# Optimization experiments

Measured on AMD Instinct MI355X. Metric: run time of the kernel, lower is better.

## Reference

```python
import jax, jax.numpy as jnp
import numpy as np

B, N, D, H, S = 4, 32768, 256, 8, 64
DH = D // H  # 32


def setup_inputs() -> dict:
    key = jax.random.key(0)
    ks = jax.random.split(key, 8)
    s = 0.02
    return {
        "x": jax.random.normal(ks[0], (B, N, D), jnp.float32),
        "W_fx": jax.random.normal(ks[1], (D, D), jnp.float32) * s,
        "b_fx": jnp.zeros((D,), jnp.float32),
        "W_x": jax.random.normal(ks[2], (D, D), jnp.float32) * s,
        "b_x": jnp.zeros((D,), jnp.float32),
        "W_slice": jax.random.normal(ks[3], (DH, S), jnp.float32) * s,
        "b_slice": jnp.zeros((S,), jnp.float32),
        "temperature": jnp.full((1, H, 1, 1), 0.5, jnp.float32),
        "W_qkv": jax.random.normal(ks[4], (DH, 3 * DH), jnp.float32) * s,  # qkv_bias=False
        "W_out": jax.random.normal(ks[5], (D, D), jnp.float32) * s,
        "b_out": jnp.zeros((D,), jnp.float32),
    }


def reference(x, W_fx, b_fx, W_x, b_x, W_slice, b_slice, temperature, W_qkv, W_out, b_out):
    b, n, d = x.shape
    h, dh = H, d // H
    scale = dh ** -0.5
    # per-head projections: [b, h, n, dh]
    fx_mid = (x @ W_fx + b_fx).reshape(b, n, h, dh).transpose(0, 2, 1, 3)
    x_mid = (x @ W_x + b_x).reshape(b, n, h, dh).transpose(0, 2, 1, 3)
    # soft slice assignment: softmax over slices [b, h, n, s]
    logits = (x_mid @ W_slice + b_slice) / temperature
    slice_weights = jax.nn.softmax(logits, axis=-1)
    slice_norm = slice_weights.sum(axis=2)  # [b, h, s]
    # weighted pooling of points into slice tokens [b, h, s, dh]
    slice_token = jnp.einsum('bhnc,bhns->bhsc', fx_mid, slice_weights)
    slice_token = slice_token / (slice_norm[..., None] + 1e-5)
    # tiny attention among slice tokens
    q, k, v = jnp.split(slice_token @ W_qkv, 3, axis=-1)
    dots = jnp.einsum('bhsc,bhtc->bhst', q, k) * scale
    attn = jax.nn.softmax(dots, axis=-1)
    out_slice_token = attn @ v  # [b, h, s, dh]
    # scatter back to points [b, h, n, dh]
    out_x = jnp.einsum('bhsc,bhns->bhnc', out_slice_token, slice_weights)
    out_x = out_x.transpose(0, 2, 1, 3).reshape(b, n, d)
    return out_x @ W_out + b_out
```

## Files before the change

### kernel.cpp

```cpp
#include <hip/hip_runtime.h>
#include <math.h>

#define TS_N 32768
#define TS_M 131072

typedef short bf16x8 __attribute__((ext_vector_type(8)));
typedef float f32x4  __attribute__((ext_vector_type(4)));
typedef unsigned short us4 __attribute__((ext_vector_type(4)));
typedef unsigned short us8 __attribute__((ext_vector_type(8)));

static __device__ __forceinline__ unsigned short f2bf(float f) {
    unsigned u = __float_as_uint(f);
    u = u + 0x7FFF + ((u >> 16) & 1);
    return (unsigned short)(u >> 16);
}
static __device__ __forceinline__ float bf2f(unsigned short b) {
    return __uint_as_float(((unsigned)b) << 16);
}

#define GL16(gp, lp) __builtin_amdgcn_global_load_lds( \
    (const __attribute__((address_space(1))) unsigned int*)(gp), \
    (__attribute__((address_space(3))) unsigned int*)(lp), 16, 0, 0)

__global__ __launch_bounds__(256) void k0_wt(
    const float* __restrict__ Wfx, const float* __restrict__ Wx,
    unsigned short* __restrict__ Wth, unsigned short* __restrict__ Wtl)
{
    const int n = blockIdx.x;
    const int wsel = blockIdx.y;
    const int k = threadIdx.x;
    const float v = (wsel ? Wx : Wfx)[k * 256 + n];
    const unsigned short hh = f2bf(v);
    const int idx = (wsel * 256 + n) * 256 + k;
    Wth[idx] = hh;
    Wtl[idx] = f2bf(v - bf2f(hh));
}

__global__ __launch_bounds__(256) void k1_gemm(
    const float* __restrict__ x,
    const unsigned short* __restrict__ Wth, const unsigned short* __restrict__ Wtl,
    const float* __restrict__ bfx, const float* __restrict__ bx,
    float* __restrict__ FX, float* __restrict__ XM)
{
    __shared__ unsigned short AldsH[4096];
    __shared__ unsigned short AldsL[4096];
    __shared__ unsigned short BldsH[4096];
    __shared__ unsigned short BldsL[4096];

    const int L = blockIdx.x;
    const int xcd = L & 7, ii = L >> 3;
    const int rb = xcd * 128 + (ii >> 2), nsel = ii & 3;
    const int row0 = rb * 128;
    const int n0 = (nsel & 1) * 128;
    const unsigned short* Bth = Wth + (nsel >> 1) * 65536 + n0 * 256;
    const unsigned short* Btl = Wtl + (nsel >> 1) * 65536 + n0 * 256;
    const float* bias = (nsel >> 1) ? bx : bfx;
    float* OUT = (nsel >> 1) ? XM : FX;

    const int t = threadIdx.x;
    const int w = t >> 6, l = t & 63;
    const int wm = w >> 1, wn = w & 1;
    const int lr = l & 15, lk = l >> 4;

    f32x4 acc[4][4];
#pragma unroll
    for (int i = 0; i < 4; ++i)
#pragma unroll
        for (int j = 0; j < 4; ++j) {
            acc[i][j][0] = 0.f; acc[i][j][1] = 0.f;
            acc[i][j][2] = 0.f; acc[i][j][3] = 0.f;
        }

    for (int step = 0; step < 8; ++step) {
        const int kk = step * 32;
        if (step > 0) __syncthreads();
#pragma unroll
        for (int g2i = 0; g2i < 2; ++g2i) {
            const int g2 = w + g2i * 4;
            const size_t br = (size_t)(g2 * 16 + lr) * 256 + kk + lk * 8;
            const int lb = g2 * 512;
            GL16(Bth + br, BldsH + lb);
            GL16(Btl + br, BldsL + lb);
        }
#pragma unroll
        for (int g2i = 0; g2i < 2; ++g2i) {
            const int g2 = w + g2i * 4;
            const float* ap = &x[(size_t)(row0 + g2 * 16 + lr) * 256 + kk + lk * 8];
            float4 a0 = *(const float4*)ap;
            float4 a1 = *(const float4*)(ap + 4);
            float cc[8] = {a0.x, a0.y, a0.z, a0.w, a1.x, a1.y, a1.z, a1.w};
            us8 vh, vl;
#pragma unroll
            for (int j = 0; j < 8; ++j) {
                const unsigned short hb = f2bf(cc[j]);
                vh[j] = hb;
                vl[j] = f2bf(cc[j] - bf2f(hb));
            }
            *(us8*)&AldsH[(g2 * 64 + l) * 8] = vh;
            *(us8*)&AldsL[(g2 * 64 + l) * 8] = vl;
        }
        __syncthreads();

        bf16x8 ah[4], al[4], bh[4], bl[4];
#pragma unroll
        for (int g = 0; g < 4; ++g) {
            const int ac = (((wm * 4 + g) * 4 + lk) * 16 + lr) * 8;
            ah[g] = *(const bf16x8*)&AldsH[ac];
            al[g] = *(const bf16x8*)&AldsL[ac];
            const int bc = (((wn * 4 + g) * 4 + lk) * 16 + lr) * 8;
            bh[g] = *(const bf16x8*)&BldsH[bc];
            bl[g] = *(const bf16x8*)&BldsL[bc];
        }
#pragma unroll
        for (int m = 0; m < 4; ++m)
#pragma unroll
            for (int n = 0; n < 4; ++n) {
                acc[m][n] = __builtin_amdgcn_mfma_f32_16x16x32_bf16(ah[m], bh[n], acc[m][n], 0, 0, 0);
                acc[m][n] = __builtin_amdgcn_mfma_f32_16x16x32_bf16(ah[m], bl[n], acc[m][n], 0, 0, 0);
                acc[m][n] = __builtin_amdgcn_mfma_f32_16x16x32_bf16(al[m], bh[n], acc[m][n], 0, 0, 0);
            }
    }

    float bv[4];
#pragma unroll
    for (int n = 0; n < 4; ++n) bv[n] = bias[n0 + wn * 64 + n * 16 + lr];
#pragma unroll
    for (int m = 0; m < 4; ++m)
#pragma unroll
        for (int n = 0; n < 4; ++n) {
            const int col = n0 + wn * 64 + n * 16 + lr;
#pragma unroll
            for (int r = 0; r < 4; ++r) {
                const int row = row0 + wm * 64 + m * 16 + lk * 4 + r;
                OUT[(size_t)row * 256 + col] = acc[m][n][r] + bv[n];
            }
        }
}

__global__ __launch_bounds__(256) void k1b_slice_softmax(
    const float* __restrict__ XM, const float* __restrict__ Wsl,
    const float* __restrict__ bsl, const float* __restrict__ temp,
    unsigned short* __restrict__ SWh, unsigned short* __restrict__ SWl)
{
    __shared__ float XMs[32][68];
    __shared__ float Ws[32][68];
    __shared__ float Ls[64][68];
    const int t  = threadIdx.x;
    const int r0 = blockIdx.x * 64;
    const int h  = blockIdx.y;

    {
        const int m = t >> 2, cq = (t & 3) * 8;
        float4 v0 = *(const float4*)&XM[(size_t)(r0 + m) * 256 + h * 32 + cq];
        float4 v1 = *(const float4*)&XM[(size_t)(r0 + m) * 256 + h * 32 + cq + 4];
        XMs[cq + 0][m] = v0.x; XMs[cq + 1][m] = v0.y; XMs[cq + 2][m] = v0.z; XMs[cq + 3][m] = v0.w;
        XMs[cq + 4][m] = v1.x; XMs[cq + 5][m] = v1.y; XMs[cq + 6][m] = v1.z; XMs[cq + 7][m] = v1.w;
        const int wk = t >> 3, wn = (t & 7) * 8;
        float4 u0 = *(const float4*)&Wsl[wk * 64 + wn];
        float4 u1 = *(const float4*)&Wsl[wk * 64 + wn + 4];
        *(float4*)&Ws[wk][wn]     = u0;
        *(float4*)&Ws[wk][wn + 4] = u1;
    }
    __syncthreads();

    const int tx = t & 15, ty = t >> 4;
    float acc[4][4];
#pragma unroll
    for (int i = 0; i < 4; ++i)
#pragma unroll
        for (int j = 0; j < 4; ++j) acc[i][j] = 0.f;
#pragma unroll
    for (int c = 0; c < 32; ++c) {
        float4 av = *(const float4*)&XMs[c][ty * 4];
        float4 bv = *(const float4*)&Ws[c][tx * 4];
        float a_[4] = {av.x, av.y, av.z, av.w};
        float b_[4] = {bv.x, bv.y, bv.z, bv.w};
#pragma unroll
        for (int i = 0; i < 4; ++i)
#pragma unroll
            for (int j = 0; j < 4; ++j)
                acc[i][j] = fmaf(a_[i], b_[j], acc[i][j]);
    }
    const float invt = 1.0f / temp[h];
#pragma unroll
    for (int i = 0; i < 4; ++i)
#pragma unroll
        for (int j = 0; j < 4; ++j)
            Ls[ty * 4 + i][tx * 4 + j] = (acc[i][j] + bsl[tx * 4 + j]) * invt;
    __syncthreads();

    const int row = t >> 2, j4 = t & 3;
    float v[16];
    float mx = -1e30f;
#pragma unroll
    for (int i = 0; i < 16; ++i) { v[i] = Ls[row][j4 * 16 + i]; mx = fmaxf(mx, v[i]); }
    mx = fmaxf(mx, __shfl_xor(mx, 1));
    mx = fmaxf(mx, __shfl_xor(mx, 2));
    float sum = 0.f;
#pragma unroll
    for (int i = 0; i < 16; ++i) { v[i] = expf(v[i] - mx); sum += v[i]; }
    sum += __shfl_xor(sum, 1);
    sum += __shfl_xor(sum, 2);
    const float inv = 1.0f / sum;
#pragma unroll
    for (int q = 0; q < 4; ++q) {
        us4 oh, ol;
#pragma unroll
        for (int j = 0; j < 4; ++j) {
            const float o = v[q * 4 + j] * inv;
            const unsigned short hh = f2bf(o);
            oh[j] = hh;
            ol[j] = f2bf(o - bf2f(hh));
        }
        const size_t idx = (size_t)(r0 + row) * 512 + h * 64 + j4 * 16 + q * 4;
        *(us4*)&SWh[idx] = oh;
        *(us4*)&SWl[idx] = ol;
    }
}

__global__ __launch_bounds__(256) void k4_gemm(
    const unsigned short* __restrict__ SWh, const unsigned short* __restrict__ SWl,
    const unsigned short* __restrict__ Gth, const unsigned short* __restrict__ Gtl,
    const float* __restrict__ bout, float* __restrict__ out)
{
    __shared__ unsigned short Alds[2][128 * 32];
    __shared__ unsigned short Blds[2][128 * 32];
    const int L = blockIdx.x;
    const int xcd = L & 7, ii = L >> 3;
    const int rb = xcd * 128 + (ii >> 1), nsel = ii & 1;
    const int row0 = rb * 128;
    const int n0 = nsel * 128;
    const int b = row0 >> 15;
    const unsigned short* Bth = Gth + ((size_t)b * 256 + n0) * 512;
    const unsigned short* Btl = Gtl + ((size_t)b * 256 + n0) * 512;

    const int t = threadIdx.x;
    const int w = t >> 6, l = t & 63;
    const int wm = w >> 1, wn = w & 1;
    const int lr = l & 15, lk = l >> 4;

    f32x4 acc[4][4];
#pragma unroll
    for (int i = 0; i < 4; ++i)
#pragma unroll
        for (int j = 0; j < 4; ++j) {
            acc[i][j][0] = 0.f; acc[i][j][1] = 0.f;
            acc[i][j][2] = 0.f; acc[i][j][3] = 0.f;
        }

    for (int step = 0; step < 16; ++step) {
        const int kk = step * 32;
        if (step > 0) __syncthreads();
#pragma unroll
        for (int g2i = 0; g2i < 2; ++g2i) {
            const int g2 = w + g2i * 4;
            const size_t ar = (size_t)(row0 + g2 * 16 + lr) * 512 + kk + lk * 8;
            const size_t br = (size_t)(g2 * 16 + lr) * 512 + kk + lk * 8;
            const int lb = g2 * 512;
            GL16(SWh + ar, &Alds[0][lb]);
            GL16(SWl + ar, &Alds[1][lb]);
            GL16(Bth + br, &Blds[0][lb]);
            GL16(Btl + br, &Blds[1][lb]);
        }
        __syncthreads();

        bf16x8 ah[4], al[4], bh[4], bl[4];
#pragma unroll
        for (int g = 0; g < 4; ++g) {
            const int ac = (((wm * 4 + g) * 4 + lk) * 16 + lr) * 8;
            ah[g] = *(const bf16x8*)&Alds[0][ac];
            al[g] = *(const bf16x8*)&Alds[1][ac];
            const int bc = (((wn * 4 + g) * 4 + lk) * 16 + lr) * 8;
            bh[g] = *(const bf16x8*)&Blds[0][bc];
            bl[g] = *(const bf16x8*)&Blds[1][bc];
        }
#pragma unroll
        for (int m = 0; m < 4; ++m)
#pragma unroll
            for (int n = 0; n < 4; ++n) {
                acc[m][n] = __builtin_amdgcn_mfma_f32_16x16x32_bf16(ah[m], bh[n], acc[m][n], 0, 0, 0);
                acc[m][n] = __builtin_amdgcn_mfma_f32_16x16x32_bf16(ah[m], bl[n], acc[m][n], 0, 0, 0);
                acc[m][n] = __builtin_amdgcn_mfma_f32_16x16x32_bf16(al[m], bh[n], acc[m][n], 0, 0, 0);
            }
    }

    float bv[4];
#pragma unroll
    for (int n = 0; n < 4; ++n) bv[n] = bout[n0 + wn * 64 + n * 16 + lr];
#pragma unroll
    for (int m = 0; m < 4; ++m)
#pragma unroll
        for (int n = 0; n < 4; ++n) {
            const int col = n0 + wn * 64 + n * 16 + lr;
#pragma unroll
            for (int r = 0; r < 4; ++r) {
                const int row = row0 + wm * 64 + m * 16 + lk * 4 + r;
                out[(size_t)row * 256 + col] = acc[m][n][r] + bv[n];
            }
        }
}

__global__ __launch_bounds__(256) void k2_pool(
    const float* __restrict__ FX,
    const unsigned short* __restrict__ SWh, const unsigned short* __restrict__ SWl,
    float* __restrict__ PART, float* __restrict__ PARTN)
{
    __shared__ float SWs[2][64][68];
    __shared__ float FXs[2][64][36];
    const int t = threadIdx.x;
    const int chunk = blockIdx.x;
    const int bh = blockIdx.y;
    const int b = bh >> 3, h = bh & 7;
    const int gbase = b * TS_N + chunk * 512;

    const int rs = t >> 2;
    const int ch0 = t & 3;

    us8 swh[2], swl[2];
    float4 fxr[2];

    {
        const size_t swbase = (size_t)(gbase + rs) * 512 + h * 64;
        swh[0] = *(const us8*)&SWh[swbase + ch0 * 8];
        swh[1] = *(const us8*)&SWh[swbase + (ch0 + 4) * 8];
        swl[0] = *(const us8*)&SWl[swbase + ch0 * 8];
        swl[1] = *(const us8*)&SWl[swbase + (ch0 + 4) * 8];
        const size_t fxbase = (size_t)(gbase + rs) * 256 + h * 32;
        fxr[0] = *(const float4*)&FX[fxbase + ch0 * 4];
        fxr[1] = *(const float4*)&FX[fxbase + (ch0 + 4) * 4];
    }

    const int c = t & 31, sb = (t >> 5) * 8;
    float acc[8];
#pragma unroll
    for (int j = 0; j < 8; ++j) acc[j] = 0.f;
    float accn = 0.f;
    int buf = 0;

    for (int s = 0; s < 8; ++s) {
#pragma unroll
        for (int q = 0; q < 2; ++q) {
            const int cq = (ch0 + q * 4) * 8;
#pragma unroll
            for (int j = 0; j < 8; ++j)
                SWs[buf][rs][cq + j] = bf2f(swh[q][j]) + bf2f(swl[q][j]);
            *(float4*)&FXs[buf][rs][(ch0 + q * 4) * 4] = fxr[q];
        }
        __syncthreads();
        if (s < 7) {
            const int g2 = gbase + (s + 1) * 64 + rs;
            const size_t swbase = (size_t)g2 * 512 + h * 64;
            swh[0] = *(const us8*)&SWh[swbase + ch0 * 8];
            swh[1] = *(const us8*)&SWh[swbase + (ch0 + 4) * 8];
            swl[0] = *(const us8*)&SWl[swbase + ch0 * 8];
            swl[1] = *(const us8*)&SWl[swbase + (ch0 + 4) * 8];
            const size_t fxbase = (size_t)g2 * 256 + h * 32;
            fxr[0] = *(const float4*)&FX[fxbase + ch0 * 4];
            fxr[1] = *(const float4*)&FX[fxbase + (ch0 + 4) * 4];
        }
#pragma unroll 8
        for (int rr = 0; rr < 64; ++rr) {
            const float f = FXs[buf][rr][c];
            float4 s0 = *(const float4*)&SWs[buf][rr][sb];
            float4 s1 = *(const float4*)&SWs[buf][rr][sb + 4];
            acc[0] = fmaf(f, s0.x, acc[0]); acc[1] = fmaf(f, s0.y, acc[1]);
            acc[2] = fmaf(f, s0.z, acc[2]); acc[3] = fmaf(f, s0.w, acc[3]);
            acc[4] = fmaf(f, s1.x, acc[4]); acc[5] = fmaf(f, s1.y, acc[5]);
            acc[6] = fmaf(f, s1.z, acc[6]); acc[7] = fmaf(f, s1.w, acc[7]);
        }
        if (t < 64) {
#pragma unroll 8
            for (int rr = 0; rr < 64; ++rr) accn += SWs[buf][rr][t];
        }
        buf ^= 1;
    }

    const int pbase = (bh * 64 + chunk) * 2048;
#pragma unroll
    for (int j = 0; j < 8; ++j) PART[pbase + (sb + j) * 32 + c] = acc[j];
    if (t < 64) PARTN[(bh * 64 + chunk) * 64 + t] = accn;
}

__global__ __launch_bounds__(256) void k2b_reduce(
    const float* __restrict__ PART, const float* __restrict__ PARTN,
    float* __restrict__ ST, float* __restrict__ NORM)
{
    const int g = blockIdx.x, bh = blockIdx.y, t = threadIdx.x;
    const int e = g * 256 + t;
    float s = 0.f;
    for (int ch = 0; ch < 64; ++ch) s += PART[(size_t)(bh * 64 + ch) * 2048 + e];
    ST[bh * 2048 + e] = s;
    if (g == 0 && t < 64) {
        float sn = 0.f;
        for (int ch = 0; ch < 64; ++ch) sn += PARTN[(bh * 64 + ch) * 64 + t];
        NORM[bh * 64 + t] = sn;
    }
}

__global__ __launch_bounds__(64) void k3_attn(
    const float* __restrict__ ST, const float* __restrict__ NORM,
    const float* __restrict__ Wqkv, float* __restrict__ OST)
{
    __shared__ float Wq[32 * 96];
    __shared__ float Kl[64][32];
    __shared__ float Vl[64][32];
    __shared__ float Dl[64][68];
    const int bh = blockIdx.x;
    const int s  = threadIdx.x;

    for (int i = 0; i < 48; ++i) Wq[i * 64 + s] = Wqkv[i * 64 + s];
    float st[32];
    const float nrm = NORM[bh * 64 + s] + 1e-5f;
#pragma unroll
    for (int c = 0; c < 32; ++c) st[c] = ST[bh * 2048 + s * 32 + c] / nrm;
    __syncthreads();

    float q[32];
#pragma unroll
    for (int o4 = 0; o4 < 8; ++o4) {
        float ax = 0.f, ay = 0.f, az = 0.f, aw = 0.f;
#pragma unroll
        for (int c = 0; c < 32; ++c) {
            float4 w = *(const float4*)&Wq[c * 96 + o4 * 4];
            ax = fmaf(st[c], w.x, ax); ay = fmaf(st[c], w.y, ay);
            az = fmaf(st[c], w.z, az); aw = fmaf(st[c], w.w, aw);
        }
        q[o4 * 4 + 0] = ax; q[o4 * 4 + 1] = ay; q[o4 * 4 + 2] = az; q[o4 * 4 + 3] = aw;
    }
#pragma unroll
    for (int o4 = 0; o4 < 8; ++o4) {
        float ax = 0.f, ay = 0.f, az = 0.f, aw = 0.f;
#pragma unroll
        for (int c = 0; c < 32; ++c) {
            float4 w = *(const float4*)&Wq[c * 96 + 32 + o4 * 4];
            ax = fmaf(st[c], w.x, ax); ay = fmaf(st[c], w.y, ay);
            az = fmaf(st[c], w.z, az); aw = fmaf(st[c], w.w, aw);
        }
        float4 kv; kv.x = ax; kv.y = ay; kv.z = az; kv.w = aw;
        *(float4*)&Kl[s][o4 * 4] = kv;
    }
#pragma unroll
    for (int o4 = 0; o4 < 8; ++o4) {
        float ax = 0.f, ay = 0.f, az = 0.f, aw = 0.f;
#pragma unroll
        for (int c = 0; c < 32; ++c) {
            float4 w = *(const float4*)&Wq[c * 96 + 64 + o4 * 4];
            ax = fmaf(st[c], w.x, ax); ay = fmaf(st[c], w.y, ay);
            az = fmaf(st[c], w.z, az); aw = fmaf(st[c], w.w, aw);
        }
        float4 vv; vv.x = ax; vv.y = ay; vv.z = az; vv.w = aw;
        *(float4*)&Vl[s][o4 * 4] = vv;
    }
    __syncthreads();

    const float scale = 0.17677669529663687f;
    float mx = -1e30f;
    for (int t2 = 0; t2 < 64; ++t2) {
        float d = 0.f;
#pragma unroll
        for (int c4 = 0; c4 < 8; ++c4) {
            float4 kv = *(const float4*)&Kl[t2][c4 * 4];
            d = fmaf(q[c4 * 4 + 0], kv.x, d); d = fmaf(q[c4 * 4 + 1], kv.y, d);
            d = fmaf(q[c4 * 4 + 2], kv.z, d); d = fmaf(q[c4 * 4 + 3], kv.w, d);
        }
        d *= scale;
        Dl[s][t2] = d;
        mx = fmaxf(mx, d);
    }
    float sum = 0.f;
    for (int t2 = 0; t2 < 64; ++t2) { float e = expf(Dl[s][t2] - mx); Dl[s][t2] = e; sum += e; }
    const float inv = 1.0f / sum;
    float out[32];
#pragma unroll
    for (int c = 0; c < 32; ++c) out[c] = 0.f;
    for (int t2 = 0; t2 < 64; ++t2) {
        const float p = Dl[s][t2] * inv;
#pragma unroll
        for (int c4 = 0; c4 < 8; ++c4) {
            float4 vv = *(const float4*)&Vl[t2][c4 * 4];
            out[c4 * 4 + 0] = fmaf(p, vv.x, out[c4 * 4 + 0]);
            out[c4 * 4 + 1] = fmaf(p, vv.y, out[c4 * 4 + 1]);
            out[c4 * 4 + 2] = fmaf(p, vv.z, out[c4 * 4 + 2]);
            out[c4 * 4 + 3] = fmaf(p, vv.w, out[c4 * 4 + 3]);
        }
    }
#pragma unroll
    for (int c4 = 0; c4 < 8; ++c4) {
        float4 ov;
        ov.x = out[c4 * 4 + 0]; ov.y = out[c4 * 4 + 1];
        ov.z = out[c4 * 4 + 2]; ov.w = out[c4 * 4 + 3];
        *(float4*)&OST[bh * 2048 + s * 32 + c4 * 4] = ov;
    }
}

__global__ __launch_bounds__(256) void k3b_precomb(
    const float* __restrict__ OST, const float* __restrict__ Wout,
    unsigned short* __restrict__ Gth, unsigned short* __restrict__ Gtl)
{
    __shared__ float OSTs[64][36];
    __shared__ float Wc[32][256];
    const int bh = blockIdx.x;
    const int b = bh >> 3, h = bh & 7;
    const int t = threadIdx.x;

#pragma unroll
    for (int j = 0; j < 2; ++j) {
        const int e = (j * 256 + t) * 4;
        float4 v = *(const float4*)&OST[bh * 2048 + e];
        const int s = e >> 5, c = e & 31;
        OSTs[s][c + 0] = v.x; OSTs[s][c + 1] = v.y;
        OSTs[s][c + 2] = v.z; OSTs[s][c + 3] = v.w;
    }
#pragma unroll
    for (int j = 0; j < 8; ++j) {
        const int e = (j * 256 + t) * 4;
        const int c = e >> 8, o = e & 255;
        *(float4*)&Wc[c][o] = *(const float4*)&Wout[(h * 32 + c) * 256 + o];
    }
    __syncthreads();

    float wcol[32];
#pragma unroll
    for (int c = 0; c < 32; ++c) wcol[c] = Wc[c][t];

    for (int s = 0; s < 64; ++s) {
        float a = 0.f;
#pragma unroll
        for (int c = 0; c < 32; ++c) a = fmaf(OSTs[s][c], wcol[c], a);
        const unsigned short gh = f2bf(a);
        const size_t idx = ((size_t)(b * 256 + t)) * 512 + h * 64 + s;
        Gth[idx] = gh;
        Gtl[idx] = f2bf(a - bf2f(gh));
    }
}

extern "C" void kernel_launch(void* const* d_in, const int* in_sizes, int n_in,
                              void* d_out, int out_size, void* d_ws, size_t ws_size,
                              hipStream_t stream) {
    (void)in_sizes; (void)n_in; (void)out_size; (void)ws_size;
    const float* x    = (const float*)d_in[0];
    const float* Wfx  = (const float*)d_in[1];
    const float* bfx  = (const float*)d_in[2];
    const float* Wx   = (const float*)d_in[3];
    const float* bx   = (const float*)d_in[4];
    const float* Wsl  = (const float*)d_in[5];
    const float* bsl  = (const float*)d_in[6];
    const float* temp = (const float*)d_in[7];
    const float* Wqkv = (const float*)d_in[8];
    const float* Wout = (const float*)d_in[9];
    const float* bout = (const float*)d_in[10];
    float* out = (float*)d_out;
    char* w = (char*)d_ws;

    float* XM = (float*)w;
    unsigned short* SWh = (unsigned short*)(w + 134217728);
    unsigned short* SWl = SWh + 67108864;
    char* p = w + 134217728 + 268435456;
    float* ST    = (float*)p;            p += 262144;
    float* NORM  = (float*)p;            p += 8192;
    float* OST   = (float*)p;            p += 262144;
    unsigned short* Gth = (unsigned short*)p; p += 1048576;
    unsigned short* Gtl = (unsigned short*)p; p += 1048576;
    unsigned short* Wth = (unsigned short*)p; p += 262144;
    unsigned short* Wtl = (unsigned short*)p; p += 262144;
    float* PART  = XM;
    float* PARTN = XM + 4194304;
    float* FX = out;

    k0_wt<<<dim3(256, 2), 256, 0, stream>>>(Wfx, Wx, Wth, Wtl);
    k1_gemm<<<4096, 256, 0, stream>>>(x, Wth, Wtl, bfx, bx, FX, XM);
    k1b_slice_softmax<<<dim3(TS_M / 64, 8), 256, 0, stream>>>(XM, Wsl, bsl, temp, SWh, SWl);
    k2_pool<<<dim3(64, 32), 256, 0, stream>>>(FX, SWh, SWl, PART, PARTN);
    k2b_reduce<<<dim3(8, 32), 256, 0, stream>>>(PART, PARTN, ST, NORM);
    k3_attn<<<32, 64, 0, stream>>>(ST, NORM, Wqkv, OST);
    k3b_precomb<<<32, 256, 0, stream>>>(OST, Wout, Gth, Gtl);
    k4_gemm<<<2048, 256, 0, stream>>>(SWh, SWl, Gth, Gtl, bout, out);
}
```

Before: 625.0 us.

## Fuse slice-logit softmax into pooling kernel to avoid re-reading slice weights

Merges the slice-logit GEMM and softmax into the pooling kernel. Each block computes slice weights for its rows, writes the bf16 hi/lo split for the later scatter GEMM, and accumulates the pooled tokens from shared memory in the same pass. This removes one kernel launch and the global re-read of the split slice weights. In exchange, the grid shrinks to 32 chunks per head, double buffering is dropped in favour of extra barriers, and PART moves to its own workspace region, so parallelism and latency hiding may drop.

```diff
diff --git a/kernel.cpp b/kernel.cpp
--- a/kernel.cpp
+++ b/kernel.cpp
@@ -137,84 +137,282 @@
         }
 }
 
-__global__ __launch_bounds__(256) void k1b_slice_softmax(
-    const float* __restrict__ XM, const float* __restrict__ Wsl,
-    const float* __restrict__ bsl, const float* __restrict__ temp,
-    unsigned short* __restrict__ SWh, unsigned short* __restrict__ SWl)
-{
-    __shared__ float XMs[32][68];
-    __shared__ float Ws[32][68];
-    __shared__ float Ls[64][68];
-    const int t  = threadIdx.x;
-    const int r0 = blockIdx.x * 64;
-    const int h  = blockIdx.y;
-
+__global__ __launch_bounds__(256) void k2_pool(
+    const float* __restrict__ FX, const float* __restrict__ XM,
+    const float* __restrict__ Wsl, const float* __restrict__ bsl,
+    const float* __restrict__ temp,
+    unsigned short* __restrict__ SWh, unsigned short* __restrict__ SWl,
+    float* __restrict__ PART, float* __restrict__ PARTN)
+{
+    __shared__ float XMs[64][36];
+    __shared__ float FXs[64][36];
+    __shared__ float SWs[64][68];
+    __shared__ float Wsls[2048];
+    const int t = threadIdx.x;
+    const int chunk = blockIdx.x;
+    const int bh = blockIdx.y;
+    const int b = bh >> 3, h = bh & 7;
+    const int gbase = b * TS_N + chunk * 1024;
+
+#pragma unroll
+    for (int j = 0; j < 8; ++j) Wsls[j * 256 + t] = Wsl[j * 256 + t];
+    const float invt = 1.0f / temp[h];
+
+    const int rs = t >> 2, cq = (t & 3) * 8;
+    float4 xm0, xm1, fx0, fx1;
     {
-        const int m = t >> 2, cq = (t & 3) * 8;
-        float4 v0 = *(const float4*)&XM[(size_t)(r0 + m) * 256 + h * 32 + cq];
-        float4 v1 = *(const float4*)&XM[(size_t)(r0 + m) * 256 + h * 32 + cq + 4];
-        XMs[cq + 0][m] = v0.x; XMs[cq + 1][m] = v0.y; XMs[cq + 2][m] = v0.z; XMs[cq + 3][m] = v0.w;
-        XMs[cq + 4][m] = v1.x; XMs[cq + 5][m] = v1.y; XMs[cq + 6][m] = v1.z; XMs[cq + 7][m] = v1.w;
-        const int wk = t >> 3, wn = (t & 7) * 8;
-        float4 u0 = *(const float4*)&Wsl[wk * 64 + wn];
-        float4 u1 = *(const float4*)&Wsl[wk * 64 + wn + 4];
-        *(float4*)&Ws[wk][wn]     = u0;
-        *(float4*)&Ws[wk][wn + 4] = u1;
-    }
+        const size_t base = (size_t)(gbase + rs) * 256 + h * 32 + cq;
+        xm0 = *(const float4*)&XM[base];
+        xm1 = *(const float4*)&XM[base + 4];
+        fx0 = *(const float4*)&FX[base];
+        fx1 = *(const float4*)&FX[base + 4];
+    }
+
+    const int c = t & 31, sb2 = (t >> 5) * 8;
+    const int row = t >> 2, p = t & 3;
+    float acc[8];
+#pragma unroll
+    for (int j = 0; j < 8; ++j) acc[j] = 0.f;
+    float accn = 0.f;
+
+    for (int s = 0; s < 16; ++s) {
+        *(float4*)&XMs[rs][cq]     = xm0;
+        *(float4*)&XMs[rs][cq + 4] = xm1;
+        *(float4*)&FXs[rs][cq]     = fx0;
+        *(float4*)&FXs[rs][cq + 4] = fx1;
+        __syncthreads();
+        if (s < 15) {
+            const size_t base = (size_t)(gbase + (s + 1) * 64 + rs) * 256 + h * 32 + cq;
+            xm0 = *(const float4*)&XM[base];
+            xm1 = *(const float4*)&XM[base + 4];
+            fx0 = *(const float4*)&FX[base];
+            fx1 = *(const float4*)&FX[base + 4];
+        }
+
+        float xm[32];
+#pragma unroll
+        for (int c2 = 0; c2 < 32; ++c2) xm[c2] = XMs[row][c2];
+        float v[16];
+        float mx = -1e30f;
+#pragma unroll
+        for (int q = 0; q < 4; ++q) {
+            float4 a = *(const float4*)&bsl[p * 16 + q * 4];
+#pragma unroll
+            for (int c2 = 0; c2 < 32; ++c2) {
+                const float4 wv = *(const float4*)&Wsls[c2 * 64 + p * 16 + q * 4];
+                a.x = fmaf(xm[c2], wv.x, a.x);
+                a.y = fmaf(xm[c2], wv.y, a.y);
+                a.z = fmaf(xm[c2], wv.z, a.z);
+                a.w = fmaf(xm[c2], wv.w, a.w);
+            }
+            float v0 = a.x * invt, v1 = a.y * invt, v2 = a.z * invt, v3 = a.w * invt;
+            v[q * 4 + 0] = v0; v[q * 4 + 1] = v1;
+            v[q * 4 + 2] = v2; v[q * 4 + 3] = v3;
+            mx = fmaxf(mx, fmaxf(fmaxf(v0, v1), fmaxf(v2, v3)));
+        }
+        mx = fmaxf(mx, __shfl_xor(mx, 1));
+        mx = fmaxf(mx, __shfl_xor(mx, 2));
+        float sum = 0.f;
+#pragma unroll
+        for (int i = 0; i < 16; ++i) { v[i] = expf(v[i] - mx); sum += v[i]; }
+        sum += __shfl_xor(sum, 1);
+        sum += __shfl_xor(sum, 2);
+        const float inv = 1.0f / sum;
+        us8 oh0, oh1, ol0, ol1;
+#pragma unroll
+        for (int j = 0; j < 8; ++j) {
+            const float o = v[j] * inv;
+            SWs[row][p * 16 + j] = o;
+            const unsigned short hb = f2bf(o);
+            oh0[j] = hb; ol0[j] = f2bf(o - bf2f(hb));
+        }
+#pragma unroll
+        for (int j = 0; j < 8; ++j) {
+            const float o = v[8 + j] * inv;
+            SWs[row][p * 16 + 8 + j] = o;
+            const unsigned short hb = f2bf(o);
+            oh1[j] = hb; ol1[j] = f2bf(o - bf2f(hb));
+        }
+        const size_t gsw = (size_t)(gbase + s * 64 + row) * 512 + h * 64 + p * 16;
+        *(us8*)&SWh[gsw]     = oh0;
+        *(us8*)&SWh[gsw + 8] = oh1;
+        *(us8*)&SWl[gsw]     = ol0;
+        *(us8*)&SWl[gsw + 8] = ol1;
+        __syncthreads();
+
+#pragma unroll 8
+        for (int rr = 0; rr < 64; ++rr) {
+            const float f = FXs[rr][c];
+            float4 s0 = *(const float4*)&SWs[rr][sb2];
+            float4 s1 = *(const float4*)&SWs[rr][sb2 + 4];
+            acc[0] = fmaf(f, s0.x, acc[0]); acc[1] = fmaf(f, s0.y, acc[1]);
+            acc[2] = fmaf(f, s0.z, acc[2]); acc[3] = fmaf(f, s0.w, acc[3]);
+            acc[4] = fmaf(f, s1.x, acc[4]); acc[5] = fmaf(f, s1.y, acc[5]);
+            acc[6] = fmaf(f, s1.z, acc[6]); acc[7] = fmaf(f, s1.w, acc[7]);
+        }
+        if (t < 64) {
+#pragma unroll 8
+            for (int rr = 0; rr < 64; ++rr) accn += SWs[rr][t];
+        }
+        __syncthreads();
+    }
+
+    const int pbase = (bh * 32 + chunk) * 2048;
+#pragma unroll
+    for (int j = 0; j < 8; ++j) PART[pbase + (sb2 + j) * 32 + c] = acc[j];
+    if (t < 64) PARTN[(bh * 32 + chunk) * 64 + t] = accn;
+}
+
+__global__ __launch_bounds__(256) void k2b_reduce(
+    const float* __restrict__ PART, const float* __restrict__ PARTN,
+    float* __restrict__ ST, float* __restrict__ NORM)
+{
+    const int g = blockIdx.x, bh = blockIdx.y, t = threadIdx.x;
+    const int e = g * 256 + t;
+    float s = 0.f;
+    for (int ch = 0; ch < 32; ++ch) s += PART[(size_t)(bh * 32 + ch) * 2048 + e];
+    ST[bh * 2048 + e] = s;
+    if (g == 0 && t < 64) {
+        float sn = 0.f;
+        for (int ch = 0; ch < 32; ++ch) sn += PARTN[(bh * 32 + ch) * 64 + t];
+        NORM[bh * 64 + t] = sn;
+    }
+}
+
+__global__ __launch_bounds__(64) void k3_attn(
+    const float* __restrict__ ST, const float* __restrict__ NORM,
+    const float* __restrict__ Wqkv, float* __restrict__ OST)
+{
+    __shared__ float Wq[32 * 96];
+    __shared__ float Kl[64][32];
+    __shared__ float Vl[64][32];
+    __shared__ float Dl[64][68];
+    const int bh = blockIdx.x;
+    const int s  = threadIdx.x;
+
+    for (int i = 0; i < 48; ++i) Wq[i * 64 + s] = Wqkv[i * 64 + s];
+    float st[32];
+    const float nrm = NORM[bh * 64 + s] + 1e-5f;
+#pragma unroll
+    for (int c = 0; c < 32; ++c) st[c] = ST[bh * 2048 + s * 32 + c] / nrm;
     __syncthreads();
 
-    const int tx = t & 15, ty = t >> 4;
-    float acc[4][4];
-#pragma unroll
-    for (int i = 0; i < 4; ++i)
-#pragma unroll
-        for (int j = 0; j < 4; ++j) acc[i][j] = 0.f;
-#pragma unroll
-    for (int c = 0; c < 32; ++c) {
-        float4 av = *(const float4*)&XMs[c][ty * 4];
-        float4 bv = *(const float4*)&Ws[c][tx * 4];
-        float a_[4] = {av.x, av.y, av.z, av.w};
-        float b_[4] = {bv.x, bv.y, bv.z, bv.w};
-#pragma unroll
-        for (int i = 0; i < 4; ++i)
-#pragma unroll
-            for (int j = 0; j < 4; ++j)
-                acc[i][j] = fmaf(a_[i], b_[j], acc[i][j]);
-    }
-    const float invt = 1.0f / temp[h];
-#pragma unroll
-    for (int i = 0; i < 4; ++i)
-#pragma unroll
-        for (int j = 0; j < 4; ++j)
-            Ls[ty * 4 + i][tx * 4 + j] = (acc[i][j] + bsl[tx * 4 + j]) * invt;
+    float q[32];
+#pragma unroll
+    for (int o4 = 0; o4 < 8; ++o4) {
+        float ax = 0.f, ay = 0.f, az = 0.f, aw = 0.f;
+#pragma unroll
+        for (int c = 0; c < 32; ++c) {
+            float4 w = *(const float4*)&Wq[c * 96 + o4 * 4];
+            ax = fmaf(st[c], w.x, ax); ay = fmaf(st[c], w.y, ay);
+            az = fmaf(st[c], w.z, az); aw = fmaf(st[c], w.w, aw);
+        }
+        q[o4 * 4 + 0] = ax; q[o4 * 4 + 1] = ay; q[o4 * 4 + 2] = az; q[o4 * 4 + 3] = aw;
+    }
+#pragma unroll
+    for (int o4 = 0; o4 < 8; ++o4) {
+        float ax = 0.f, ay = 0.f, az = 0.f, aw = 0.f;
+#pragma unroll
+        for (int c = 0; c < 32; ++c) {
+            float4 w = *(const float4*)&Wq[c * 96 + 32 + o4 * 4];
+            ax = fmaf(st[c], w.x, ax); ay = fmaf(st[c], w.y, ay);
+            az = fmaf(st[c], w.z, az); aw = fmaf(st[c], w.w, aw);
+        }
+        float4 kv; kv.x = ax; kv.y = ay; kv.z = az; kv.w = aw;
+        *(float4*)&Kl[s][o4 * 4] = kv;
+    }
+#pragma unroll
+    for (int o4 = 0; o4 < 8; ++o4) {
+        float ax = 0.f, ay = 0.f, az = 0.f, aw = 0.f;
+#pragma unroll
+        for (int c = 0; c < 32; ++c) {
+            float4 w = *(const float4*)&Wq[c * 96 + 64 + o4 * 4];
+            ax = fmaf(st[c], w.x, ax); ay = fmaf(st[c], w.y, ay);
+            az = fmaf(st[c], w.z, az); aw = fmaf(st[c], w.w, aw);
+        }
+        float4 vv; vv.x = ax; vv.y = ay; vv.z = az; vv.w = aw;
+        *(float4*)&Vl[s][o4 * 4] = vv;
+    }
     __syncthreads();
 
-    const int row = t >> 2, j4 = t & 3;
-    float v[16];
+    const float scale = 0.17677669529663687f;
     float mx = -1e30f;
-#pragma unroll
-    for (int i = 0; i < 16; ++i) { v[i] = Ls[row][j4 * 16 + i]; mx = fmaxf(mx, v[i]); }
-    mx = fmaxf(mx, __shfl_xor(mx, 1));
-    mx = fmaxf(mx, __shfl_xor(mx, 2));
+    for (int t2 = 0; t2 < 64; ++t2) {
+        float d = 0.f;
+#pragma unroll
+        for (int c4 = 0; c4 < 8; ++c4) {
+            float4 kv = *(const float4*)&Kl[t2][c4 * 4];
+            d = fmaf(q[c4 * 4 + 0], kv.x, d); d = fmaf(q[c4 * 4 + 1], kv.y, d);
+            d = fmaf(q[c4 * 4 + 2], kv.z, d); d = fmaf(q[c4 * 4 + 3], kv.w, d);
+        }
+        d *= scale;
+        Dl[s][t2] = d;
+        mx = fmaxf(mx, d);
+    }
     float sum = 0.f;
-#pragma unroll
-    for (int i = 0; i < 16; ++i) { v[i] = expf(v[i] - mx); sum += v[i]; }
-    sum += __shfl_xor(sum, 1);
-    sum += __shfl_xor(sum, 2);
+    for (int t2 = 0; t2 < 64; ++t2) { float e = expf(Dl[s][t2] - mx); Dl[s][t2] = e; sum += e; }
     const float inv = 1.0f / sum;
-#pragma unroll
-    for (int q = 0; q < 4; ++q) {
-        us4 oh, ol;
-#pragma unroll
-        for (int j = 0; j < 4; ++j) {
-            const float o = v[q * 4 + j] * inv;
-            const unsigned short hh = f2bf(o);
-            oh[j] = hh;
-            ol[j] = f2bf(o - bf2f(hh));
-        }
-        const size_t idx = (size_t)(r0 + row) * 512 + h * 64 + j4 * 16 + q * 4;
-        *(us4*)&SWh[idx] = oh;
-        *(us4*)&SWl[idx] = ol;
+    float out[32];
+#pragma unroll
+    for (int c = 0; c < 32; ++c) out[c] = 0.f;
+    for (int t2 = 0; t2 < 64; ++t2) {
+        const float p = Dl[s][t2] * inv;
+#pragma unroll
+        for (int c4 = 0; c4 < 8; ++c4) {
+            float4 vv = *(const float4*)&Vl[t2][c4 * 4];
+            out[c4 * 4 + 0] = fmaf(p, vv.x, out[c4 * 4 + 0]);
+            out[c4 * 4 + 1] = fmaf(p, vv.y, out[c4 * 4 + 1]);
+            out[c4 * 4 + 2] = fmaf(p, vv.z, out[c4 * 4 + 2]);
+            out[c4 * 4 + 3] = fmaf(p, vv.w, out[c4 * 4 + 3]);
+        }
+    }
+#pragma unroll
+    for (int c4 = 0; c4 < 8; ++c4) {
+        float4 ov;
+        ov.x = out[c4 * 4 + 0]; ov.y = out[c4 * 4 + 1];
+        ov.z = out[c4 * 4 + 2]; ov.w = out[c4 * 4 + 3];
+        *(float4*)&OST[bh * 2048 + s * 32 + c4 * 4] = ov;
+    }
+}
+
+__global__ __launch_bounds__(256) void k3b_precomb(
+    const float* __restrict__ OST, const float* __restrict__ Wout,
+    unsigned short* __restrict__ Gth, unsigned short* __restrict__ Gtl)
+{
+    __shared__ float OSTs[64][36];
+    __shared__ float Wc[32][256];
+    const int bh = blockIdx.x;
+    const int b = bh >> 3, h = bh & 7;
+    const int t = threadIdx.x;
+
+#pragma unroll
+    for (int j = 0; j < 2; ++j) {
+        const int e = (j * 256 + t) * 4;
+        float4 v = *(const float4*)&OST[bh * 2048 + e];
+        const int s = e >> 5, c = e & 31;
+        OSTs[s][c + 0] = v.x; OSTs[s][c + 1] = v.y;
+        OSTs[s][c + 2] = v.z; OSTs[s][c + 3] = v.w;
+    }
+#pragma unroll
+    for (int j = 0; j < 8; ++j) {
+        const int e = (j * 256 + t) * 4;
+        const int c = e >> 8, o = e & 255;
+        *(float4*)&Wc[c][o] = *(const float4*)&Wout[(h * 32 + c) * 256 + o];
+    }
+    __syncthreads();
+
+    float wcol[32];
+#pragma unroll
+    for (int c = 0; c < 32; ++c) wcol[c] = Wc[c][t];
+
+    for (int s = 0; s < 64; ++s) {
+        float a = 0.f;
+#pragma unroll
+        for (int c = 0; c < 32; ++c) a = fmaf(OSTs[s][c], wcol[c], a);
+        const unsigned short gh = f2bf(a);
+        const size_t idx = ((size_t)(b * 256 + t)) * 512 + h * 64 + s;
+        Gth[idx] = gh;
+        Gtl[idx] = f2bf(a - bf2f(gh));
     }
 }
 
@@ -298,240 +496,6 @@
                 out[(size_t)row * 256 + col] = acc[m][n][r] + bv[n];
             }
         }
-}
-
-__global__ __launch_bounds__(256) void k2_pool(
-    const float* __restrict__ FX,
-    const unsigned short* __restrict__ SWh, const unsigned short* __restrict__ SWl,
-    float* __restrict__ PART, float* __restrict__ PARTN)
-{
-    __shared__ float SWs[2][64][68];
-    __shared__ float FXs[2][64][36];
-    const int t = threadIdx.x;
-    const int chunk = blockIdx.x;
-    const int bh = blockIdx.y;
-    const int b = bh >> 3, h = bh & 7;
-    const int gbase = b * TS_N + chunk * 512;
-
-    const int rs = t >> 2;
-    const int ch0 = t & 3;
-
-    us8 swh[2], swl[2];
-    float4 fxr[2];
-
-    {
-        const size_t swbase = (size_t)(gbase + rs) * 512 + h * 64;
-        swh[0] = *(const us8*)&SWh[swbase + ch0 * 8];
-        swh[1] = *(const us8*)&SWh[swbase + (ch0 + 4) * 8];
-        swl[0] = *(const us8*)&SWl[swbase + ch0 * 8];
-        swl[1] = *(const us8*)&SWl[swbase + (ch0 + 4) * 8];
-        const size_t fxbase = (size_t)(gbase + rs) * 256 + h * 32;
-        fxr[0] = *(const float4*)&FX[fxbase + ch0 * 4];
-        fxr[1] = *(const float4*)&FX[fxbase + (ch0 + 4) * 4];
-    }
-
-    const int c = t & 31, sb = (t >> 5) * 8;
-    float acc[8];
-#pragma unroll
-    for (int j = 0; j < 8; ++j) acc[j] = 0.f;
-    float accn = 0.f;
-    int buf = 0;
-
-    for (int s = 0; s < 8; ++s) {
-#pragma unroll
-        for (int q = 0; q < 2; ++q) {
-            const int cq = (ch0 + q * 4) * 8;
-#pragma unroll
-            for (int j = 0; j < 8; ++j)
-                SWs[buf][rs][cq + j] = bf2f(swh[q][j]) + bf2f(swl[q][j]);
-            *(float4*)&FXs[buf][rs][(ch0 + q * 4) * 4] = fxr[q];
-        }
-        __syncthreads();
-        if (s < 7) {
-            const int g2 = gbase + (s + 1) * 64 + rs;
-            const size_t swbase = (size_t)g2 * 512 + h * 64;
-            swh[0] = *(const us8*)&SWh[swbase + ch0 * 8];
-            swh[1] = *(const us8*)&SWh[swbase + (ch0 + 4) * 8];
-            swl[0] = *(const us8*)&SWl[swbase + ch0 * 8];
-            swl[1] = *(const us8*)&SWl[swbase + (ch0 + 4) * 8];
-            const size_t fxbase = (size_t)g2 * 256 + h * 32;
-            fxr[0] = *(const float4*)&FX[fxbase + ch0 * 4];
-            fxr[1] = *(const float4*)&FX[fxbase + (ch0 + 4) * 4];
-        }
-#pragma unroll 8
-        for (int rr = 0; rr < 64; ++rr) {
-            const float f = FXs[buf][rr][c];
-            float4 s0 = *(const float4*)&SWs[buf][rr][sb];
-            float4 s1 = *(const float4*)&SWs[buf][rr][sb + 4];
-            acc[0] = fmaf(f, s0.x, acc[0]); acc[1] = fmaf(f, s0.y, acc[1]);
-            acc[2] = fmaf(f, s0.z, acc[2]); acc[3] = fmaf(f, s0.w, acc[3]);
-            acc[4] = fmaf(f, s1.x, acc[4]); acc[5] = fmaf(f, s1.y, acc[5]);
-            acc[6] = fmaf(f, s1.z, acc[6]); acc[7] = fmaf(f, s1.w, acc[7]);
-        }
-        if (t < 64) {
-#pragma unroll 8
-            for (int rr = 0; rr < 64; ++rr) accn += SWs[buf][rr][t];
-        }
-        buf ^= 1;
-    }
-
-    const int pbase = (bh * 64 + chunk) * 2048;
-#pragma unroll
-    for (int j = 0; j < 8; ++j) PART[pbase + (sb + j) * 32 + c] = acc[j];
-    if (t < 64) PARTN[(bh * 64 + chunk) * 64 + t] = accn;
-}
-
-__global__ __launch_bounds__(256) void k2b_reduce(
-    const float* __restrict__ PART, const float* __restrict__ PARTN,
-    float* __restrict__ ST, float* __restrict__ NORM)
-{
-    const int g = blockIdx.x, bh = blockIdx.y, t = threadIdx.x;
-    const int e = g * 256 + t;
-    float s = 0.f;
-    for (int ch = 0; ch < 64; ++ch) s += PART[(size_t)(bh * 64 + ch) * 2048 + e];
-    ST[bh * 2048 + e] = s;
-    if (g == 0 && t < 64) {
-        float sn = 0.f;
-        for (int ch = 0; ch < 64; ++ch) sn += PARTN[(bh * 64 + ch) * 64 + t];
-        NORM[bh * 64 + t] = sn;
-    }
-}
-
-__global__ __launch_bounds__(64) void k3_attn(
-    const float* __restrict__ ST, const float* __restrict__ NORM,
-    const float* __restrict__ Wqkv, float* __restrict__ OST)
-{
-    __shared__ float Wq[32 * 96];
-    __shared__ float Kl[64][32];
-    __shared__ float Vl[64][32];
-    __shared__ float Dl[64][68];
-    const int bh = blockIdx.x;
-    const int s  = threadIdx.x;
-
-    for (int i = 0; i < 48; ++i) Wq[i * 64 + s] = Wqkv[i * 64 + s];
-    float st[32];
-    const float nrm = NORM[bh * 64 + s] + 1e-5f;
-#pragma unroll
-    for (int c = 0; c < 32; ++c) st[c] = ST[bh * 2048 + s * 32 + c] / nrm;
-    __syncthreads();
-
-    float q[32];
-#pragma unroll
-    for (int o4 = 0; o4 < 8; ++o4) {
-        float ax = 0.f, ay = 0.f, az = 0.f, aw = 0.f;
-#pragma unroll
-        for (int c = 0; c < 32; ++c) {
-            float4 w = *(const float4*)&Wq[c * 96 + o4 * 4];
-            ax = fmaf(st[c], w.x, ax); ay = fmaf(st[c], w.y, ay);
-            az = fmaf(st[c], w.z, az); aw = fmaf(st[c], w.w, aw);
-        }
-        q[o4 * 4 + 0] = ax; q[o4 * 4 + 1] = ay; q[o4 * 4 + 2] = az; q[o4 * 4 + 3] = aw;
-    }
-#pragma unroll
-    for (int o4 = 0; o4 < 8; ++o4) {
-        float ax = 0.f, ay = 0.f, az = 0.f, aw = 0.f;
-#pragma unroll
-        for (int c = 0; c < 32; ++c) {
-            float4 w = *(const float4*)&Wq[c * 96 + 32 + o4 * 4];
-            ax = fmaf(st[c], w.x, ax); ay = fmaf(st[c], w.y, ay);
-            az = fmaf(st[c], w.z, az); aw = fmaf(st[c], w.w, aw);
-        }
-        float4 kv; kv.x = ax; kv.y = ay; kv.z = az; kv.w = aw;
-        *(float4*)&Kl[s][o4 * 4] = kv;
-    }
-#pragma unroll
-    for (int o4 = 0; o4 < 8; ++o4) {
-        float ax = 0.f, ay = 0.f, az = 0.f, aw = 0.f;
-#pragma unroll
-        for (int c = 0; c < 32; ++c) {
-            float4 w = *(const float4*)&Wq[c * 96 + 64 + o4 * 4];
-            ax = fmaf(st[c], w.x, ax); ay = fmaf(st[c], w.y, ay);
-            az = fmaf(st[c], w.z, az); aw = fmaf(st[c], w.w, aw);
-        }
-        float4 vv; vv.x = ax; vv.y = ay; vv.z = az; vv.w = aw;
-        *(float4*)&Vl[s][o4 * 4] = vv;
-    }
-    __syncthreads();
-
-    const float scale = 0.17677669529663687f;
-    float mx = -1e30f;
-    for (int t2 = 0; t2 < 64; ++t2) {
-        float d = 0.f;
-#pragma unroll
-        for (int c4 = 0; c4 < 8; ++c4) {
-            float4 kv = *(const float4*)&Kl[t2][c4 * 4];
-            d = fmaf(q[c4 * 4 + 0], kv.x, d); d = fmaf(q[c4 * 4 + 1], kv.y, d);
-            d = fmaf(q[c4 * 4 + 2], kv.z, d); d = fmaf(q[c4 * 4 + 3], kv.w, d);
-        }
-        d *= scale;
-        Dl[s][t2] = d;
-        mx = fmaxf(mx, d);
-    }
-    float sum = 0.f;
-    for (int t2 = 0; t2 < 64; ++t2) { float e = expf(Dl[s][t2] - mx); Dl[s][t2] = e; sum += e; }
-    const float inv = 1.0f / sum;
-    float out[32];
-#pragma unroll
-    for (int c = 0; c < 32; ++c) out[c] = 0.f;
-    for (int t2 = 0; t2 < 64; ++t2) {
-        const float p = Dl[s][t2] * inv;
-#pragma unroll
-        for (int c4 = 0; c4 < 8; ++c4) {
-            float4 vv = *(const float4*)&Vl[t2][c4 * 4];
-            out[c4 * 4 + 0] = fmaf(p, vv.x, out[c4 * 4 + 0]);
-            out[c4 * 4 + 1] = fmaf(p, vv.y, out[c4 * 4 + 1]);
-            out[c4 * 4 + 2] = fmaf(p, vv.z, out[c4 * 4 + 2]);
-            out[c4 * 4 + 3] = fmaf(p, vv.w, out[c4 * 4 + 3]);
-        }
-    }
-#pragma unroll
-    for (int c4 = 0; c4 < 8; ++c4) {
-        float4 ov;
-        ov.x = out[c4 * 4 + 0]; ov.y = out[c4 * 4 + 1];
-        ov.z = out[c4 * 4 + 2]; ov.w = out[c4 * 4 + 3];
-        *(float4*)&OST[bh * 2048 + s * 32 + c4 * 4] = ov;
-    }
-}
-
-__global__ __launch_bounds__(256) void k3b_precomb(
-    const float* __restrict__ OST, const float* __restrict__ Wout,
-    unsigned short* __restrict__ Gth, unsigned short* __restrict__ Gtl)
-{
-    __shared__ float OSTs[64][36];
-    __shared__ float Wc[32][256];
-    const int bh = blockIdx.x;
-    const int b = bh >> 3, h = bh & 7;
-    const int t = threadIdx.x;
-
-#pragma unroll
-    for (int j = 0; j < 2; ++j) {
-        const int e = (j * 256 + t) * 4;
-        float4 v = *(const float4*)&OST[bh * 2048 + e];
-        const int s = e >> 5, c = e & 31;
-        OSTs[s][c + 0] = v.x; OSTs[s][c + 1] = v.y;
-        OSTs[s][c + 2] = v.z; OSTs[s][c + 3] = v.w;
-    }
-#pragma unroll
-    for (int j = 0; j < 8; ++j) {
-        const int e = (j * 256 + t) * 4;
-        const int c = e >> 8, o = e & 255;
-        *(float4*)&Wc[c][o] = *(const float4*)&Wout[(h * 32 + c) * 256 + o];
-    }
-    __syncthreads();
-
-    float wcol[32];
-#pragma unroll
-    for (int c = 0; c < 32; ++c) wcol[c] = Wc[c][t];
-
-    for (int s = 0; s < 64; ++s) {
-        float a = 0.f;
-#pragma unroll
-        for (int c = 0; c < 32; ++c) a = fmaf(OSTs[s][c], wcol[c], a);
-        const unsigned short gh = f2bf(a);
-        const size_t idx = ((size_t)(b * 256 + t)) * 512 + h * 64 + s;
-        Gth[idx] = gh;
-        Gtl[idx] = f2bf(a - bf2f(gh));
-    }
 }
 
 extern "C" void kernel_launch(void* const* d_in, const int* in_sizes, int n_in,
@@ -563,14 +527,14 @@
     unsigned short* Gtl = (unsigned short*)p; p += 1048576;
     unsigned short* Wth = (unsigned short*)p; p += 262144;
     unsigned short* Wtl = (unsigned short*)p; p += 262144;
-    float* PART  = XM;
-    float* PARTN = XM + 4194304;
+    float* PART  = (float*)p;            p += 8388608;
+    float* PARTN = (float*)p;            p += 262144;
     float* FX = out;
 
     k0_wt<<<dim3(256, 2), 256, 0, stream>>>(Wfx, Wx, Wth, Wtl);
     k1_gemm<<<4096, 256, 0, stream>>>(x, Wth, Wtl, bfx, bx, FX, XM);
-    k1b_slice_softmax<<<dim3(TS_M / 64, 8), 256, 0, stream>>>(XM, Wsl, bsl, temp, SWh, SWl);
-    k2_pool<<<dim3(64, 32), 256, 0, stream>>>(FX, SWh, SWl, PART, PARTN);
+    k2_pool<<<dim3(32, 32), 256, 0, stream>>>(FX, XM, Wsl, bsl, temp,
+                                              SWh, SWl, PART, PARTN);
     k2b_reduce<<<dim3(8, 32), 256, 0, stream>>>(PART, PARTN, ST, NORM);
     k3_attn<<<32, 64, 0, stream>>>(ST, NORM, Wqkv, OST);
     k3b_precomb<<<32, 256, 0, stream>>>(OST, Wout, Gth, Gtl);
```

New measurement: 660.1 us. 5.6% more time.
